# Kernel optimization log

Measured on AMD Instinct MI355X. Metric: run time of the kernel, lower is better.

The kernel has to match this reference:

```python
import jax, jax.numpy as jnp
import numpy as np


def setup_inputs() -> dict:
    key = jax.random.key(0)
    k1, k2 = jax.random.split(key)
    B, Q, C, H, W = 2, 100, 151, 128, 128
    pred_logits = jax.random.normal(k1, (B, Q, C), dtype=jnp.float32)
    pred_masks = jax.random.normal(k2, (B, Q, H, W), dtype=jnp.float32)
    return {"pred_logits": pred_logits, "pred_masks": pred_masks, "out_size": 512}


def reference(pred_logits, pred_masks, out_size):
    B, Q, C = pred_logits.shape
    # class_scores[b,q,c] * mask_probs[b,q,h,w] summed over q == contraction bqc,bqhw->bchw
    class_scores = jax.nn.softmax(pred_logits, axis=-1)
    mask_probs = jax.nn.sigmoid(pred_masks)
    seg = jnp.einsum('bqc,bqhw->bchw', class_scores, mask_probs)
    seg = seg[:, 1:, :, :]  # drop background class 0
    # bilinear, half-pixel centers == torch align_corners=False
    seg = jax.image.resize(seg, (B, C - 1, out_size, out_size), method='bilinear')
    return seg
```

## Files before the change

kernel.cpp:

```cpp
#include <hip/hip_runtime.h>
#include <hip/hip_bf16.h>
#include <math.h>

#define NCLS 151
#define NQ   100
#define NB   2
#define HW   16384
#define NCO  150
#define OUTW 512
#define KPAD 128
#define CPAD 160
#define CBLK 32
#define AROW 136
#define BROW 136
#define SROW 130

using short8  = __attribute__((ext_vector_type(8))) short;
using short4v = __attribute__((ext_vector_type(4))) short;
using f32x4   = __attribute__((ext_vector_type(4))) float;

static __device__ __forceinline__ ushort f2bf(float x) {
    union { float f; unsigned u; } v; v.f = x;
    unsigned r = v.u + 0x7fff + ((v.u >> 16) & 1);
    return (ushort)(r >> 16);
}

__global__ __launch_bounds__(64) void softmax_k(const float* __restrict__ logits,
                                                ushort* __restrict__ scoresT) {
    int q = blockIdx.x & 127;
    int b = blockIdx.x >> 7;
    int lane = threadIdx.x;
    ushort* A = scoresT + (size_t)b * CPAD * KPAD;

    if (q >= NQ) {
        A[lane * KPAD + q] = 0;
        A[(lane + 64) * KPAD + q] = 0;
        if (lane < 32) A[(lane + 128) * KPAD + q] = 0;
        return;
    }

    const float* in = logits + (size_t)(b * NQ + q) * NCLS;
    float v0 = in[lane];
    float v1 = in[lane + 64];
    float v2 = (lane < NCLS - 128) ? in[lane + 128] : -1e30f;

    float m = fmaxf(fmaxf(v0, v1), v2);
    #pragma unroll
    for (int o = 32; o; o >>= 1) m = fmaxf(m, __shfl_xor(m, o));

    float e0 = __expf(v0 - m);
    float e1 = __expf(v1 - m);
    float e2 = (lane < NCLS - 128) ? __expf(v2 - m) : 0.f;

    float s = e0 + e1 + e2;
    #pragma unroll
    for (int o = 32; o; o >>= 1) s += __shfl_xor(s, o);

    float inv = 1.f / s;
    if (lane >= 1) A[(lane - 1) * KPAD + q] = f2bf(e0 * inv);
    A[(lane + 63) * KPAD + q] = f2bf(e1 * inv);
    if (lane < 23)       A[(lane + 127) * KPAD + q] = f2bf(e2 * inv);
    else if (lane < 33)  A[(lane + 127) * KPAD + q] = 0;
}

__global__ __launch_bounds__(1024, 1) void fused_k(const float* __restrict__ masks,
                                                   const ushort* __restrict__ scoresT,
                                                   float* __restrict__ out) {
    __shared__ __align__(16) ushort s_a[CPAD][AROW];
    __shared__ __align__(16) ushort s_bt[256][BROW];
    __shared__ float s_seg[2][CBLK][SROW];

    int r   = blockIdx.x;
    int b   = blockIdx.y;
    int tid = threadIdx.x;
    int r1  = min(r + 1, 127);
    int wid = tid >> 6, lane = tid & 63;
    int pr = lane & 15, kg = lane >> 4;

    {
        const float4* asrc = (const float4*)(scoresT + (size_t)b * CPAD * KPAD);
        #pragma unroll
        for (int j = 0; j < 2; ++j) {
            int i = tid + j * 1024;
            float4 v = asrc[i];
            *(float4*)&s_a[i >> 4][(i & 15) * 8] = v;
        }
        if (tid < 512) {
            int i = 2048 + tid;
            float4 v = asrc[i];
            *(float4*)&s_a[i >> 4][(i & 15) * 8] = v;
        }
    }

    {
        const float* mb = masks + (size_t)b * NQ * HW;
        #pragma unroll
        for (int i0 = 0; i0 < 8192; i0 += 1024) {
            int i = i0 + tid;
            int p = i & 255, kk4 = i >> 8;
            int gpix = ((p < 128) ? r : r1) * 128 + (p & 127);
            short4v sv;
            #pragma unroll
            for (int e = 0; e < 4; ++e) {
                int gk = kk4 * 4 + e;
                float s = 0.f;
                if (gk < NQ) {
                    float x = mb[(size_t)gk * HW + gpix];
                    s = 1.f / (1.f + __expf(-x));
                }
                sv[e] = (short)f2bf(s);
            }
            *(short4v*)&s_bt[p][kk4 * 4] = sv;
        }
    }
    __syncthreads();

    int pw = wid * 16;
    for (int cs = 0; cs < 5; ++cs) {
        f32x4 acc[2];
        acc[0] = (f32x4){0.f, 0.f, 0.f, 0.f};
        acc[1] = (f32x4){0.f, 0.f, 0.f, 0.f};

        #pragma unroll
        for (int ks = 0; ks < 4; ++ks) {
            short8 bf = *(const short8*)&s_bt[pw + pr][ks * 32 + kg * 8];
            #pragma unroll
            for (int ct = 0; ct < 2; ++ct) {
                short8 af = *(const short8*)&s_a[cs * CBLK + ct * 16 + pr][ks * 32 + kg * 8];
                acc[ct] = __builtin_amdgcn_mfma_f32_16x16x32_bf16(af, bf, acc[ct], 0, 0, 0);
            }
        }

        __syncthreads();

        {
            int p = pw + pr, rs = p >> 7, px = p & 127;
            #pragma unroll
            for (int ct = 0; ct < 2; ++ct)
                #pragma unroll
                for (int j = 0; j < 4; ++j)
                    s_seg[rs][ct * 16 + kg * 4 + j][px] = acc[ct][j];
        }
        __syncthreads();

        int cbase = cs * CBLK;
        for (int it = tid; it < CBLK * 128; it += 1024) {
            int k = it & 127;
            int c = it >> 7;
            int cg = cbase + c;
            if (cg >= NCO) break;
            int km = max(k - 1, 0), kp = min(k + 1, 127);
            const float* s0 = s_seg[0][c];
            const float* s1 = s_seg[1][c];
            float a0 = s0[km], a1 = s0[k], a2 = s0[kp];
            float b0 = s1[km], b1 = s1[k], b2 = s1[kp];

            float t0 = a0 + 0.625f * (a1 - a0);
            float t1 = a0 + 0.875f * (a1 - a0);
            float t2 = a1 + 0.125f * (a2 - a1);
            float t3 = a1 + 0.375f * (a2 - a1);
            float u0 = b0 + 0.625f * (b1 - b0);
            float u1 = b0 + 0.875f * (b1 - b0);
            float u2 = b1 + 0.125f * (b2 - b1);
            float u3 = b1 + 0.375f * (b2 - b1);

            float* op = out + (size_t)(b * NCO + cg) * (OUTW * OUTW) + 4 * k;

            if (r == 0) {
                f32x4 o = {t0, t1, t2, t3};
                *(f32x4*)(op) = o;
                *(f32x4*)(op + OUTW) = o;
            }
            int nr = (r == 127) ? 2 : 4;
            #pragma unroll
            for (int ri = 0; ri < 4; ++ri) {
                if (ri >= nr) break;
                float fh = 0.125f + 0.25f * (float)ri;
                int h = 4 * r + 2 + ri;
                f32x4 o;
                o.x = t0 + fh * (u0 - t0);
                o.y = t1 + fh * (u1 - t1);
                o.z = t2 + fh * (u2 - t2);
                o.w = t3 + fh * (u3 - t3);
                *(f32x4*)(op + (size_t)h * OUTW) = o;
            }
        }
    }
}

extern "C" void kernel_launch(void* const* d_in, const int* in_sizes, int n_in,
                              void* d_out, int out_size, void* d_ws, size_t ws_size,
                              hipStream_t stream) {
    const float* logits = (const float*)d_in[0];
    const float* masks  = (const float*)d_in[1];
    float* out = (float*)d_out;

    ushort* scoresT = (ushort*)d_ws;

    softmax_k<<<dim3(NB * 128), dim3(64), 0, stream>>>(logits, scoresT);
    fused_k<<<dim3(128, NB), dim3(1024), 0, stream>>>(masks, scoresT, out);
}
```

Before: 68.40 us.

## Fuse softmax into main kernel and use nontemporal mask loads

Removes the separate softmax kernel and workspace round trip. Each block now computes the class softmax for its batch directly into shared memory after zeroing the padded tile. This eliminates a kernel launch and the global scoresT transfer, at the cost of redundant softmax work in every block. Mask loads are also marked nontemporal.

```diff
diff --git a/kernel.cpp b/kernel.cpp
--- a/kernel.cpp
+++ b/kernel.cpp
@@ -25,46 +25,8 @@
     return (ushort)(r >> 16);
 }
 
-__global__ __launch_bounds__(64) void softmax_k(const float* __restrict__ logits,
-                                                ushort* __restrict__ scoresT) {
-    int q = blockIdx.x & 127;
-    int b = blockIdx.x >> 7;
-    int lane = threadIdx.x;
-    ushort* A = scoresT + (size_t)b * CPAD * KPAD;
-
-    if (q >= NQ) {
-        A[lane * KPAD + q] = 0;
-        A[(lane + 64) * KPAD + q] = 0;
-        if (lane < 32) A[(lane + 128) * KPAD + q] = 0;
-        return;
-    }
-
-    const float* in = logits + (size_t)(b * NQ + q) * NCLS;
-    float v0 = in[lane];
-    float v1 = in[lane + 64];
-    float v2 = (lane < NCLS - 128) ? in[lane + 128] : -1e30f;
-
-    float m = fmaxf(fmaxf(v0, v1), v2);
-    #pragma unroll
-    for (int o = 32; o; o >>= 1) m = fmaxf(m, __shfl_xor(m, o));
-
-    float e0 = __expf(v0 - m);
-    float e1 = __expf(v1 - m);
-    float e2 = (lane < NCLS - 128) ? __expf(v2 - m) : 0.f;
-
-    float s = e0 + e1 + e2;
-    #pragma unroll
-    for (int o = 32; o; o >>= 1) s += __shfl_xor(s, o);
-
-    float inv = 1.f / s;
-    if (lane >= 1) A[(lane - 1) * KPAD + q] = f2bf(e0 * inv);
-    A[(lane + 63) * KPAD + q] = f2bf(e1 * inv);
-    if (lane < 23)       A[(lane + 127) * KPAD + q] = f2bf(e2 * inv);
-    else if (lane < 33)  A[(lane + 127) * KPAD + q] = 0;
-}
-
-__global__ __launch_bounds__(1024, 1) void fused_k(const float* __restrict__ masks,
-                                                   const ushort* __restrict__ scoresT,
+__global__ __launch_bounds__(1024, 1) void fused_k(const float* __restrict__ logits,
+                                                   const float* __restrict__ masks,
                                                    float* __restrict__ out) {
     __shared__ __align__(16) ushort s_a[CPAD][AROW];
     __shared__ __align__(16) ushort s_bt[256][BROW];
@@ -78,18 +40,9 @@
     int pr = lane & 15, kg = lane >> 4;
 
     {
-        const float4* asrc = (const float4*)(scoresT + (size_t)b * CPAD * KPAD);
-        #pragma unroll
-        for (int j = 0; j < 2; ++j) {
-            int i = tid + j * 1024;
-            float4 v = asrc[i];
-            *(float4*)&s_a[i >> 4][(i & 15) * 8] = v;
-        }
-        if (tid < 512) {
-            int i = 2048 + tid;
-            float4 v = asrc[i];
-            *(float4*)&s_a[i >> 4][(i & 15) * 8] = v;
-        }
+        float4 z = {0.f, 0.f, 0.f, 0.f};
+        for (int i = tid; i < CPAD * 17; i += 1024)
+            *(float4*)&s_a[i / 17][(i % 17) * 8] = z;
     }
 
     {
@@ -105,12 +58,44 @@
                 int gk = kk4 * 4 + e;
                 float s = 0.f;
                 if (gk < NQ) {
-                    float x = mb[(size_t)gk * HW + gpix];
+                    float x = __builtin_nontemporal_load(&mb[(size_t)gk * HW + gpix]);
                     s = 1.f / (1.f + __expf(-x));
                 }
                 sv[e] = (short)f2bf(s);
             }
             *(short4v*)&s_bt[p][kk4 * 4] = sv;
+        }
+    }
+    __syncthreads();
+
+    {
+        int grp = lane >> 3, e = lane & 7;
+        int q = wid * 8 + grp;
+        if (q < NQ) {
+            const float* in = logits + (size_t)(b * NQ + q) * NCLS;
+            float v[19];
+            float m = -1e30f;
+            #pragma unroll
+            for (int i = 0; i < 19; ++i) {
+                int c = e + 8 * i;
+                v[i] = (c < NCLS) ? in[c] : -1e30f;
+                m = fmaxf(m, v[i]);
+            }
+            m = fmaxf(m, __shfl_xor(m, 1));
+            m = fmaxf(m, __shfl_xor(m, 2));
+            m = fmaxf(m, __shfl_xor(m, 4));
+            float s = 0.f;
+            #pragma unroll
+            for (int i = 0; i < 19; ++i) { v[i] = __expf(v[i] - m); s += v[i]; }
+            s += __shfl_xor(s, 1);
+            s += __shfl_xor(s, 2);
+            s += __shfl_xor(s, 4);
+            float inv = 1.f / s;
+            #pragma unroll
+            for (int i = 0; i < 19; ++i) {
+                int c = e + 8 * i;
+                if (c >= 1 && c < NCLS) s_a[c - 1][q] = f2bf(v[i] * inv);
+            }
         }
     }
     __syncthreads();
@@ -195,8 +180,5 @@
     const float* masks  = (const float*)d_in[1];
     float* out = (float*)d_out;
 
-    ushort* scoresT = (ushort*)d_ws;
-
-    softmax_k<<<dim3(NB * 128), dim3(64), 0, stream>>>(logits, scoresT);
-    fused_k<<<dim3(128, NB), dim3(1024), 0, stream>>>(masks, scoresT, out);
+    fused_k<<<dim3(128, NB), dim3(1024), 0, stream>>>(logits, masks, out);
 }
```

Result: faster. 59.43 us (-13.1%).
